# Kernel optimization log

Hardware: AMD Instinct MI355X
Metric: run time of the kernel (lower is better)

## Reference

```python
import jax, jax.numpy as jnp
import numpy as np

DIMS = (50000, 50000)
ORDER = len(DIMS)
NUM_FEATS = 64
QLEVEL = 4
Q = 1 << QLEVEL
V = 1 << ORDER                      # number of corners (2^order)
N_QUERIES = 1_000_000
WHICH_AXIS = np.repeat(np.arange(ORDER), DIMS)          # [sum(dims)]
OFFSETS = np.concatenate([[0], np.cumsum(DIMS)[:-1]])   # row offset of each axis in feats
# corner bit table: flattening of a [2]*order grid is row-major, so axis i's bit is (v >> (ORDER-1-i)) & 1
VBITS = (np.arange(V)[:, None] >> (ORDER - 1 - np.arange(ORDER))[None, :]) & 1  # [V, ORDER]


def setup_inputs() -> dict:
    key = jax.random.key(0)
    k = jax.random.split(key, 8)
    S = sum(DIMS)
    init_scale = 0.01 / NUM_FEATS ** 0.5
    values = jax.random.truncated_normal(k[0], -2.0, 2.0, (1, V, NUM_FEATS), dtype=jnp.float32) * init_scale
    feats = jax.random.uniform(k[1], (S, NUM_FEATS), dtype=jnp.float32)
    lo = 1.0 / (1 << (QLEVEL + 1))
    cand_row = jnp.linspace(lo, 1.0 - lo, Q, dtype=jnp.float32).reshape(1, 1, Q)
    candidates = jnp.tile(cand_row, (ORDER, NUM_FEATS, 1))
    scale = jnp.zeros((1,), jnp.float32)
    bias = jnp.zeros((1,), jnp.float32)
    idx0 = jax.random.randint(k[2], (N_QUERIES,), 0, DIMS[0])
    idx1 = jax.random.randint(k[3], (N_QUERIES,), 0, DIMS[1])
    return {"values": values, "feats": feats, "candidates": candidates,
            "scale": scale, "bias": bias, "idx0": idx0, "idx1": idx1}


def reference(values, feats, candidates, scale, bias, idx0, idx1):
    # --- prepare_inputs: straight-through quantization of feats ---
    target_keys = candidates[WHICH_AXIS]                                  # [S, F, Q]
    assigned = jnp.argmin(jnp.abs(feats[:, :, None] - target_keys), -1)   # [S, F]
    qkeys = jnp.take_along_axis(target_keys, assigned[:, :, None], -1)[..., 0]  # [S, F]
    probs = qkeys + feats - jax.lax.stop_gradient(feats)                  # STE
    p = jnp.stack([probs, 1.0 - probs], 0)                                # [2, S, F]

    # --- per-axis gathers ---
    idxs = [idx0, idx1]
    gathers = [p[:, OFFSETS[i] + idxs[i]] for i in range(ORDER)]          # each [2, N, F]

    # --- corner-wise outer product across axes ---
    corner = gathers[0][VBITS[:, 0]]                                      # [V, N, F]
    for i in range(1, ORDER):
        corner = corner * gathers[i][VBITS[:, i]]

    # --- contraction with corner values, halve features, tanh gate ---
    t = jnp.einsum('vf,vnf->nf', values[0], corner)                       # [N, F]
    half = NUM_FEATS // 2
    a = t[:, :half].sum(-1)                                               # [N]
    b = t[:, half:].sum(-1)                                               # [N]
    return a * jnp.tanh(b) * jnp.exp(scale[0]) + bias[0]
```

## Files before the change

### kernel.cpp

```cpp
#include <hip/hip_runtime.h>
#include <stdint.h>

#define NF    64
#define DIM0  50000
#define SROWS 100000
#define TPB   256
#define QPT   2
#define COEF_OFF_BYTES (SROWS * 32)

typedef float    f32x4 __attribute__((ext_vector_type(4)));
typedef uint32_t u32x4 __attribute__((ext_vector_type(4)));

__global__ void quantize_kernel(const float* __restrict__ feats,
                                const float* __restrict__ values,
                                uint32_t* __restrict__ qcodes,
                                float* __restrict__ coef) {
    int t = threadIdx.x;
    if (blockIdx.x == 0 && t < NF) {
        float v0 = values[t], v1 = values[NF + t];
        float v2 = values[2 * NF + t], v3 = values[3 * NF + t];
        float W = v0 - v1 - v2 + v3;
        float X = v1 - v3, Y = v2 - v3;
        float Wp = W * (1.0f / 256.0f);
        float Xp = W * (1.0f / 512.0f) + X * (1.0f / 16.0f);
        float Yp = W * (1.0f / 512.0f) + Y * (1.0f / 16.0f);
        float C  = W * (1.0f / 1024.0f) + (X + Y) * (1.0f / 32.0f) + v3;
        ((f32x4*)coef)[t] = (f32x4){Wp, Xp, Yp, C};
        float Cs = C;
        Cs += __shfl_xor(Cs, 1);  Cs += __shfl_xor(Cs, 2);
        Cs += __shfl_xor(Cs, 4);  Cs += __shfl_xor(Cs, 8);
        Cs += __shfl_xor(Cs, 16);
        if (t == 0)  coef[NF * 4 + 0] = Cs;
        if (t == 32) coef[NF * 4 + 1] = Cs;
    }

    int gid = blockIdx.x * blockDim.x + t;
    const f32x4* fr = (const f32x4*)(feats + (size_t)gid * 8);
    f32x4 fA = __builtin_nontemporal_load(fr);
    f32x4 fB = __builtin_nontemporal_load(fr + 1);
    float fv[8] = {fA.x, fA.y, fA.z, fA.w, fB.x, fB.y, fB.z, fB.w};

    uint32_t word = 0u;
#pragma unroll
    for (int j = 0; j < 8; ++j) {
        float x = fmaf(fv[j], 16.0f, -1.0f);
        int q = (int)ceilf(x);
        q = q < 0 ? 0 : (q > 15 ? 15 : q);
        word |= (uint32_t)q << (4 * j);
    }
    __builtin_nontemporal_store(word, qcodes + gid);
}

__global__ __launch_bounds__(TPB) void query_kernel(
        const uint32_t* __restrict__ qcodes,
        const f32x4* __restrict__ coef,
        const float* __restrict__ scale,
        const float* __restrict__ bias,
        const int* __restrict__ idx0,
        const int* __restrict__ idx1,
        float* __restrict__ out, int N) {
    int t = threadIdx.x;
    int base = blockIdx.x * (TPB * QPT) + t;

    uint32_t aw[QPT][8], bw[QPT][8];
#pragma unroll
    for (int k = 0; k < QPT; ++k) {
        int n = base + k * TPB;
        int m = n < N ? n : N - 1;
        int r0 = __builtin_nontemporal_load(idx0 + m);
        int r1 = DIM0 + __builtin_nontemporal_load(idx1 + m);
        const u32x4* pa = (const u32x4*)(qcodes + (size_t)r0 * 8);
        const u32x4* pb = (const u32x4*)(qcodes + (size_t)r1 * 8);
        u32x4 x0 = pa[0], x1 = pa[1];
        u32x4 y0 = pb[0], y1 = pb[1];
        aw[k][0] = x0.x; aw[k][1] = x0.y; aw[k][2] = x0.z; aw[k][3] = x0.w;
        aw[k][4] = x1.x; aw[k][5] = x1.y; aw[k][6] = x1.z; aw[k][7] = x1.w;
        bw[k][0] = y0.x; bw[k][1] = y0.y; bw[k][2] = y0.z; bw[k][3] = y0.w;
        bw[k][4] = y1.x; bw[k][5] = y1.y; bw[k][6] = y1.z; bw[k][7] = y1.w;
    }

    float a1[QPT] = {0.f, 0.f};
    float b1[QPT] = {0.f, 0.f};
#pragma unroll
    for (int wd = 0; wd < 8; ++wd) {
#pragma unroll
        for (int j = 0; j < 8; ++j) {
            int f = wd * 8 + j;
            f32x4 c = coef[f];
#pragma unroll
            for (int k = 0; k < QPT; ++k) {
                float A = (float)((aw[k][wd] >> (4 * j)) & 15u);
                float B = (float)((bw[k][wd] >> (4 * j)) & 15u);
                float h = fmaf(c.x, B, c.y);
                float g = fmaf(c.z, B, (wd < 4 ? a1[k] : b1[k]));
                if (wd < 4) a1[k] = fmaf(A, h, g);
                else        b1[k] = fmaf(A, h, g);
            }
        }
    }

    const float* cs = (const float*)coef;
    float Ca = cs[NF * 4 + 0];
    float Cb = cs[NF * 4 + 1];
    float es = expf(scale[0]);
    float bi = bias[0];
#pragma unroll
    for (int k = 0; k < QPT; ++k) {
        int n = base + k * TPB;
        if (n < N) {
            float asum = a1[k] + Ca;
            float bsum = b1[k] + Cb;
            __builtin_nontemporal_store(asum * tanhf(bsum) * es + bi, out + n);
        }
    }
}

extern "C" void kernel_launch(void* const* d_in, const int* in_sizes, int n_in,
                              void* d_out, int out_size, void* d_ws, size_t ws_size,
                              hipStream_t stream) {
    const float* values = (const float*)d_in[0];
    const float* feats  = (const float*)d_in[1];
    const float* scale  = (const float*)d_in[3];
    const float* bias   = (const float*)d_in[4];
    const int*   idx0   = (const int*)d_in[5];
    const int*   idx1   = (const int*)d_in[6];
    float*       out    = (float*)d_out;

    uint32_t* qcodes = (uint32_t*)d_ws;
    float*    coef   = (float*)((char*)d_ws + COEF_OFF_BYTES);

    int nwords = SROWS * 8;
    quantize_kernel<<<nwords / TPB, TPB, 0, stream>>>(feats, values, qcodes, coef);

    int N = out_size;
    int qblocks = (N + TPB * QPT - 1) / (TPB * QPT);
    query_kernel<<<qblocks, TPB, 0, stream>>>(
        qcodes, (const f32x4*)coef, scale, bias, idx0, idx1, out, N);
}
```

Measured before the change: 44.79 us.

## Bucket queries by idx0 block and stage axis-0 codes in LDS

Adds a counting sort of queries by idx0>>8: a histogram fused into the quantize kernel, a serial prefix kernel and a scatter kernel that writes packed (n, low row bits, idx1) records. The query kernel then loads 256 axis-0 code rows per bucket into LDS and serves axis-0 gathers from there, leaving only the axis-1 gather in global memory. The goal is to remove random global gathers for one axis. In exchange it adds three more launches, a memset, atomics and a record array written and read back, and the output writes become scattered.

```diff
diff --git a/kernel.cpp b/kernel.cpp
--- a/kernel.cpp
+++ b/kernel.cpp
@@ -1,117 +1,198 @@
 #include <hip/hip_runtime.h>
 #include <stdint.h>
 
-#define NF    64
-#define DIM0  50000
-#define SROWS 100000
-#define TPB   256
-#define QPT   2
-#define COEF_OFF_BYTES (SROWS * 32)
+#define NF     64
+#define DIM0   50000
+#define SROWS  100000
+#define TPB    256
+#define NB     196
+#define KSPLIT 8
+#define QBLKS  3125
+
+#define OFF_CODES 0u
+#define OFF_COEF  3200000u
+#define OFF_CNT   3201536u
+#define OFF_BASE  3202560u
+#define OFF_CUR   3203584u
+#define OFF_REC   3204608u
 
 typedef float    f32x4 __attribute__((ext_vector_type(4)));
 typedef uint32_t u32x4 __attribute__((ext_vector_type(4)));
-
-__global__ void quantize_kernel(const float* __restrict__ feats,
-                                const float* __restrict__ values,
-                                uint32_t* __restrict__ qcodes,
-                                float* __restrict__ coef) {
+typedef uint32_t u32x2 __attribute__((ext_vector_type(2)));
+
+__global__ __launch_bounds__(TPB) void quanthist_kernel(
+        const float* __restrict__ feats, const float* __restrict__ values,
+        const int* __restrict__ idx0,
+        uint32_t* __restrict__ qcodes, float* __restrict__ coef,
+        uint32_t* __restrict__ gcnt, int N) {
+    int bid = blockIdx.x;
+    int t   = threadIdx.x;
+
+    if (bid < QBLKS) {
+        if (bid == 0 && t < NF) {
+            float v0 = values[t], v1 = values[NF + t];
+            float v2 = values[2 * NF + t], v3 = values[3 * NF + t];
+            float W = v0 - v1 - v2 + v3;
+            float X = v1 - v3, Y = v2 - v3;
+            float Wp = W * (1.0f / 256.0f);
+            float Xp = W * (1.0f / 512.0f) + X * (1.0f / 16.0f);
+            float Yp = W * (1.0f / 512.0f) + Y * (1.0f / 16.0f);
+            float C  = W * (1.0f / 1024.0f) + (X + Y) * (1.0f / 32.0f) + v3;
+            ((f32x4*)coef)[t] = (f32x4){Wp, Xp, Yp, C};
+            float Cs = C;
+            Cs += __shfl_xor(Cs, 1);  Cs += __shfl_xor(Cs, 2);
+            Cs += __shfl_xor(Cs, 4);  Cs += __shfl_xor(Cs, 8);
+            Cs += __shfl_xor(Cs, 16);
+            if (t == 0)  coef[NF * 4 + 0] = Cs;
+            if (t == 32) coef[NF * 4 + 1] = Cs;
+        }
+        int gid = bid * TPB + t;
+        const f32x4* fr = (const f32x4*)(feats + (size_t)gid * 8);
+        f32x4 fA = __builtin_nontemporal_load(fr);
+        f32x4 fB = __builtin_nontemporal_load(fr + 1);
+        float fv[8] = {fA.x, fA.y, fA.z, fA.w, fB.x, fB.y, fB.z, fB.w};
+        uint32_t word = 0u;
+#pragma unroll
+        for (int j = 0; j < 8; ++j) {
+            float x = fmaf(fv[j], 16.0f, -1.0f);
+            int q = (int)ceilf(x);
+            q = q < 0 ? 0 : (q > 15 ? 15 : q);
+            word |= (uint32_t)q << (4 * j);
+        }
+        qcodes[gid] = word;
+    } else {
+        __shared__ uint32_t scnt[NB];
+        for (int i = t; i < NB; i += TPB) scnt[i] = 0;
+        __syncthreads();
+        int q0 = (bid - QBLKS) * 1024;
+#pragma unroll
+        for (int k = 0; k < 4; ++k) {
+            int n = q0 + k * TPB + t;
+            if (n < N) atomicAdd(&scnt[(uint32_t)idx0[n] >> 8], 1u);
+        }
+        __syncthreads();
+        for (int i = t; i < NB; i += TPB)
+            if (scnt[i]) atomicAdd(&gcnt[i], scnt[i]);
+    }
+}
+
+__global__ void prefix_kernel(const uint32_t* __restrict__ cnt,
+                              uint32_t* __restrict__ base,
+                              uint32_t* __restrict__ cursor) {
+    if (threadIdx.x == 0 && blockIdx.x == 0) {
+        uint32_t acc = 0;
+        for (int i = 0; i < NB; ++i) {
+            base[i] = acc; cursor[i] = acc; acc += cnt[i];
+        }
+        base[NB] = acc;
+    }
+}
+
+__global__ __launch_bounds__(TPB) void scatter_kernel(
+        const int* __restrict__ idx0, const int* __restrict__ idx1,
+        uint32_t* __restrict__ cursor, uint2* __restrict__ rec, int N) {
+    __shared__ uint32_t scnt[NB];
+    __shared__ uint32_t sstart[NB];
     int t = threadIdx.x;
-    if (blockIdx.x == 0 && t < NF) {
-        float v0 = values[t], v1 = values[NF + t];
-        float v2 = values[2 * NF + t], v3 = values[3 * NF + t];
-        float W = v0 - v1 - v2 + v3;
-        float X = v1 - v3, Y = v2 - v3;
-        float Wp = W * (1.0f / 256.0f);
-        float Xp = W * (1.0f / 512.0f) + X * (1.0f / 16.0f);
-        float Yp = W * (1.0f / 512.0f) + Y * (1.0f / 16.0f);
-        float C  = W * (1.0f / 1024.0f) + (X + Y) * (1.0f / 32.0f) + v3;
-        ((f32x4*)coef)[t] = (f32x4){Wp, Xp, Yp, C};
-        float Cs = C;
-        Cs += __shfl_xor(Cs, 1);  Cs += __shfl_xor(Cs, 2);
-        Cs += __shfl_xor(Cs, 4);  Cs += __shfl_xor(Cs, 8);
-        Cs += __shfl_xor(Cs, 16);
-        if (t == 0)  coef[NF * 4 + 0] = Cs;
-        if (t == 32) coef[NF * 4 + 1] = Cs;
-    }
-
-    int gid = blockIdx.x * blockDim.x + t;
-    const f32x4* fr = (const f32x4*)(feats + (size_t)gid * 8);
-    f32x4 fA = __builtin_nontemporal_load(fr);
-    f32x4 fB = __builtin_nontemporal_load(fr + 1);
-    float fv[8] = {fA.x, fA.y, fA.z, fA.w, fB.x, fB.y, fB.z, fB.w};
-
-    uint32_t word = 0u;
-#pragma unroll
-    for (int j = 0; j < 8; ++j) {
-        float x = fmaf(fv[j], 16.0f, -1.0f);
-        int q = (int)ceilf(x);
-        q = q < 0 ? 0 : (q > 15 ? 15 : q);
-        word |= (uint32_t)q << (4 * j);
-    }
-    __builtin_nontemporal_store(word, qcodes + gid);
-}
-
-__global__ __launch_bounds__(TPB) void query_kernel(
+    for (int i = t; i < NB; i += TPB) scnt[i] = 0;
+    __syncthreads();
+
+    int q0 = blockIdx.x * 1024;
+    int r0v[4], r1v[4], bk[4];
+#pragma unroll
+    for (int k = 0; k < 4; ++k) {
+        int n = q0 + k * TPB + t;
+        if (n < N) {
+            r0v[k] = __builtin_nontemporal_load(idx0 + n);
+            r1v[k] = __builtin_nontemporal_load(idx1 + n);
+            bk[k] = (uint32_t)r0v[k] >> 8;
+            atomicAdd(&scnt[bk[k]], 1u);
+        } else bk[k] = -1;
+    }
+    __syncthreads();
+    for (int i = t; i < NB; i += TPB) {
+        uint32_t c = scnt[i];
+        sstart[i] = c ? atomicAdd(&cursor[i], c) : 0u;
+    }
+    __syncthreads();
+    for (int i = t; i < NB; i += TPB) scnt[i] = 0;
+    __syncthreads();
+#pragma unroll
+    for (int k = 0; k < 4; ++k) {
+        if (bk[k] >= 0) {
+            int n = q0 + k * TPB + t;
+            uint32_t r = atomicAdd(&scnt[bk[k]], 1u);
+            uint32_t pos = sstart[bk[k]] + r;
+            rec[pos] = make_uint2((uint32_t)n | ((uint32_t)(r0v[k] & 255) << 20),
+                                  (uint32_t)r1v[k]);
+        }
+    }
+}
+
+__global__ __launch_bounds__(TPB) void bquery_kernel(
         const uint32_t* __restrict__ qcodes,
+        const uint2* __restrict__ rec,
+        const uint32_t* __restrict__ base,
         const f32x4* __restrict__ coef,
         const float* __restrict__ scale,
         const float* __restrict__ bias,
-        const int* __restrict__ idx0,
-        const int* __restrict__ idx1,
-        float* __restrict__ out, int N) {
+        float* __restrict__ out) {
+    __shared__ uint32_t lds[256 * 8];
+    int b = blockIdx.x / KSPLIT;
+    int k = blockIdx.x % KSPLIT;
     int t = threadIdx.x;
-    int base = blockIdx.x * (TPB * QPT) + t;
-
-    uint32_t aw[QPT][8], bw[QPT][8];
-#pragma unroll
-    for (int k = 0; k < QPT; ++k) {
-        int n = base + k * TPB;
-        int m = n < N ? n : N - 1;
-        int r0 = __builtin_nontemporal_load(idx0 + m);
-        int r1 = DIM0 + __builtin_nontemporal_load(idx1 + m);
-        const u32x4* pa = (const u32x4*)(qcodes + (size_t)r0 * 8);
-        const u32x4* pb = (const u32x4*)(qcodes + (size_t)r1 * 8);
-        u32x4 x0 = pa[0], x1 = pa[1];
-        u32x4 y0 = pb[0], y1 = pb[1];
-        aw[k][0] = x0.x; aw[k][1] = x0.y; aw[k][2] = x0.z; aw[k][3] = x0.w;
-        aw[k][4] = x1.x; aw[k][5] = x1.y; aw[k][6] = x1.z; aw[k][7] = x1.w;
-        bw[k][0] = y0.x; bw[k][1] = y0.y; bw[k][2] = y0.z; bw[k][3] = y0.w;
-        bw[k][4] = y1.x; bw[k][5] = y1.y; bw[k][6] = y1.z; bw[k][7] = y1.w;
-    }
-
-    float a1[QPT] = {0.f, 0.f};
-    float b1[QPT] = {0.f, 0.f};
-#pragma unroll
-    for (int wd = 0; wd < 8; ++wd) {
-#pragma unroll
-        for (int j = 0; j < 8; ++j) {
-            int f = wd * 8 + j;
-            f32x4 c = coef[f];
-#pragma unroll
-            for (int k = 0; k < QPT; ++k) {
-                float A = (float)((aw[k][wd] >> (4 * j)) & 15u);
-                float B = (float)((bw[k][wd] >> (4 * j)) & 15u);
-                float h = fmaf(c.x, B, c.y);
-                float g = fmaf(c.z, B, (wd < 4 ? a1[k] : b1[k]));
-                if (wd < 4) a1[k] = fmaf(A, h, g);
-                else        b1[k] = fmaf(A, h, g);
-            }
-        }
-    }
-
+
+    int row0  = b * 256;
+    int nrows = min(256, DIM0 - row0);
+    int words = nrows * 8;
+    for (int i = t; i < words; i += TPB)
+        lds[i] = qcodes[(size_t)row0 * 8 + i];
+
+    uint32_t s = base[b], e = base[b + 1];
+    __syncthreads();
+
+    uint32_t len   = e - s;
+    uint32_t chunk = (len + KSPLIT - 1) / KSPLIT;
+    uint32_t start = s + (uint32_t)k * chunk;
+    uint32_t end   = min(start + chunk, e);
+
+    float es = expf(scale[0]);
+    float bi = bias[0];
     const float* cs = (const float*)coef;
     float Ca = cs[NF * 4 + 0];
     float Cb = cs[NF * 4 + 1];
-    float es = expf(scale[0]);
-    float bi = bias[0];
-#pragma unroll
-    for (int k = 0; k < QPT; ++k) {
-        int n = base + k * TPB;
-        if (n < N) {
-            float asum = a1[k] + Ca;
-            float bsum = b1[k] + Cb;
-            __builtin_nontemporal_store(asum * tanhf(bsum) * es + bi, out + n);
-        }
+
+    for (uint32_t i = start + t; i < end; i += TPB) {
+        u32x2 rc = __builtin_nontemporal_load((const u32x2*)(rec + i));
+        uint32_t n    = rc.x & 0xFFFFFu;
+        uint32_t r0lo = (rc.x >> 20) & 0xFFu;
+        uint32_t r1   = rc.y;
+
+        const uint32_t* ar = &lds[r0lo * 8];
+        uint32_t aw[8];
+#pragma unroll
+        for (int w = 0; w < 8; ++w) aw[w] = ar[w];
+        const u32x4* pb = (const u32x4*)(qcodes + ((size_t)DIM0 + r1) * 8);
+        u32x4 y0 = pb[0], y1 = pb[1];
+        uint32_t bw[8] = {y0.x, y0.y, y0.z, y0.w, y1.x, y1.y, y1.z, y1.w};
+
+        float a1 = 0.f, b1 = 0.f;
+#pragma unroll
+        for (int wd = 0; wd < 8; ++wd) {
+#pragma unroll
+            for (int j = 0; j < 8; ++j) {
+                int f = wd * 8 + j;
+                f32x4 c = coef[f];
+                float A = (float)((aw[wd] >> (4 * j)) & 15u);
+                float B = (float)((bw[wd] >> (4 * j)) & 15u);
+                float h = fmaf(c.x, B, c.y);
+                float g = fmaf(c.z, B, (wd < 4 ? a1 : b1));
+                if (wd < 4) a1 = fmaf(A, h, g);
+                else        b1 = fmaf(A, h, g);
+            }
+        }
+        float res = (a1 + Ca) * tanhf(b1 + Cb) * es + bi;
+        __builtin_nontemporal_store(res, out + n);
     }
 }
 
@@ -126,14 +207,22 @@
     const int*   idx1   = (const int*)d_in[6];
     float*       out    = (float*)d_out;
 
-    uint32_t* qcodes = (uint32_t*)d_ws;
-    float*    coef   = (float*)((char*)d_ws + COEF_OFF_BYTES);
-
-    int nwords = SROWS * 8;
-    quantize_kernel<<<nwords / TPB, TPB, 0, stream>>>(feats, values, qcodes, coef);
+    char* ws = (char*)d_ws;
+    uint32_t* qcodes = (uint32_t*)(ws + OFF_CODES);
+    float*    coef   = (float*)   (ws + OFF_COEF);
+    uint32_t* gcnt   = (uint32_t*)(ws + OFF_CNT);
+    uint32_t* gbase  = (uint32_t*)(ws + OFF_BASE);
+    uint32_t* gcur   = (uint32_t*)(ws + OFF_CUR);
+    uint2*    rec    = (uint2*)   (ws + OFF_REC);
 
     int N = out_size;
-    int qblocks = (N + TPB * QPT - 1) / (TPB * QPT);
-    query_kernel<<<qblocks, TPB, 0, stream>>>(
-        qcodes, (const f32x4*)coef, scale, bias, idx0, idx1, out, N);
-}
+    int hblks = (N + 1023) / 1024;
+
+    hipMemsetAsync(gcnt, 0, NB * sizeof(uint32_t), stream);
+    quanthist_kernel<<<QBLKS + hblks, TPB, 0, stream>>>(
+        feats, values, idx0, qcodes, coef, gcnt, N);
+    prefix_kernel<<<1, 64, 0, stream>>>(gcnt, gbase, gcur);
+    scatter_kernel<<<hblks, TPB, 0, stream>>>(idx0, idx1, gcur, rec, N);
+    bquery_kernel<<<NB * KSPLIT, TPB, 0, stream>>>(
+        qcodes, rec, gbase, (const f32x4*)coef, scale, bias, out);
+}
```

Measured after the change: 112.1 us. 2.5x slower.

## Bucket queries by idx0 range before gathering to improve cache locality

Applied to the files above, without the earlier changes.

Adds a scatter pass that sorts queries into 8 buckets by idx0 row range, writing packed (query id, r0, r1) records. The query kernel then processes each bucket in chunks so the idx0-side code rows in flight stay within a small slice, aiming for better L2/MALL reuse. In exchange it adds a memset, an extra kernel launch, a global atomic and a write plus read of 8 MB of records, and the output writes become scattered. The qcodes table is only about 3.2 MB, so it may already fit in cache.

```diff
diff --git a/kernel.cpp b/kernel.cpp
--- a/kernel.cpp
+++ b/kernel.cpp
@@ -1,20 +1,27 @@
 #include <hip/hip_runtime.h>
 #include <stdint.h>
 
-#define NF    64
-#define DIM0  50000
-#define SROWS 100000
-#define TPB   256
-#define QPT   2
-#define COEF_OFF_BYTES (SROWS * 32)
+#define NF     64
+#define DIM0   50000
+#define SROWS  100000
+#define TPB    256
+#define NBKT   8
+#define BROWS  6250
+#define CAP    160000u
+#define NCH    512
+#define QBLKS  3125
+
+#define OFF_CODES 0u
+#define OFF_COEF  3200000u
+#define OFF_CUR   3202048u
+#define OFF_REC   3203072u
 
 typedef float    f32x4 __attribute__((ext_vector_type(4)));
 typedef uint32_t u32x4 __attribute__((ext_vector_type(4)));
 
-__global__ void quantize_kernel(const float* __restrict__ feats,
-                                const float* __restrict__ values,
-                                uint32_t* __restrict__ qcodes,
-                                float* __restrict__ coef) {
+__global__ __launch_bounds__(TPB) void quantize_kernel(
+        const float* __restrict__ feats, const float* __restrict__ values,
+        uint32_t* __restrict__ qcodes, float* __restrict__ coef) {
     int t = threadIdx.x;
     if (blockIdx.x == 0 && t < NF) {
         float v0 = values[t], v1 = values[NF + t];
@@ -34,7 +41,7 @@
         if (t == 32) coef[NF * 4 + 1] = Cs;
     }
 
-    int gid = blockIdx.x * blockDim.x + t;
+    int gid = blockIdx.x * TPB + t;
     const f32x4* fr = (const f32x4*)(feats + (size_t)gid * 8);
     f32x4 fA = __builtin_nontemporal_load(fr);
     f32x4 fB = __builtin_nontemporal_load(fr + 1);
@@ -48,70 +55,96 @@
         q = q < 0 ? 0 : (q > 15 ? 15 : q);
         word |= (uint32_t)q << (4 * j);
     }
-    __builtin_nontemporal_store(word, qcodes + gid);
+    qcodes[gid] = word;
 }
 
-__global__ __launch_bounds__(TPB) void query_kernel(
+__global__ __launch_bounds__(TPB) void scatter_kernel(
+        const int* __restrict__ idx0, const int* __restrict__ idx1,
+        uint32_t* __restrict__ cursor, uint2* __restrict__ rec, int N) {
+    __shared__ uint32_t scnt[NBKT], sstart[NBKT];
+    int t = threadIdx.x;
+    if (t < NBKT) scnt[t] = 0;
+    __syncthreads();
+
+    int q0 = blockIdx.x * 1024;
+    int r0v[4], r1v[4], bk[4];
+    uint32_t rk[4];
+#pragma unroll
+    for (int k = 0; k < 4; ++k) {
+        int n = q0 + k * TPB + t;
+        if (n < N) {
+            r0v[k] = __builtin_nontemporal_load(idx0 + n);
+            r1v[k] = __builtin_nontemporal_load(idx1 + n);
+            bk[k]  = (uint32_t)r0v[k] / BROWS;
+            rk[k]  = atomicAdd(&scnt[bk[k]], 1u);
+        } else bk[k] = -1;
+    }
+    __syncthreads();
+    if (t < NBKT) sstart[t] = scnt[t] ? atomicAdd(&cursor[t], scnt[t]) : 0u;
+    __syncthreads();
+#pragma unroll
+    for (int k = 0; k < 4; ++k) {
+        if (bk[k] >= 0) {
+            int n = q0 + k * TPB + t;
+            uint32_t pos = (uint32_t)bk[k] * CAP + sstart[bk[k]] + rk[k];
+            rec[pos] = make_uint2((uint32_t)n,
+                                  ((uint32_t)r0v[k] << 16) | (uint32_t)r1v[k]);
+        }
+    }
+}
+
+__global__ __launch_bounds__(TPB) void bquery_kernel(
         const uint32_t* __restrict__ qcodes,
+        const uint2* __restrict__ rec,
+        const uint32_t* __restrict__ cursor,
         const f32x4* __restrict__ coef,
         const float* __restrict__ scale,
         const float* __restrict__ bias,
-        const int* __restrict__ idx0,
-        const int* __restrict__ idx1,
-        float* __restrict__ out, int N) {
-    int t = threadIdx.x;
-    int base = blockIdx.x * (TPB * QPT) + t;
+        float* __restrict__ out) {
+    int b  = blockIdx.x & (NBKT - 1);
+    int ch = blockIdx.x >> 3;
 
-    uint32_t aw[QPT][8], bw[QPT][8];
-#pragma unroll
-    for (int k = 0; k < QPT; ++k) {
-        int n = base + k * TPB;
-        int m = n < N ? n : N - 1;
-        int r0 = __builtin_nontemporal_load(idx0 + m);
-        int r1 = DIM0 + __builtin_nontemporal_load(idx1 + m);
-        const u32x4* pa = (const u32x4*)(qcodes + (size_t)r0 * 8);
-        const u32x4* pb = (const u32x4*)(qcodes + (size_t)r1 * 8);
-        u32x4 x0 = pa[0], x1 = pa[1];
-        u32x4 y0 = pb[0], y1 = pb[1];
-        aw[k][0] = x0.x; aw[k][1] = x0.y; aw[k][2] = x0.z; aw[k][3] = x0.w;
-        aw[k][4] = x1.x; aw[k][5] = x1.y; aw[k][6] = x1.z; aw[k][7] = x1.w;
-        bw[k][0] = y0.x; bw[k][1] = y0.y; bw[k][2] = y0.z; bw[k][3] = y0.w;
-        bw[k][4] = y1.x; bw[k][5] = y1.y; bw[k][6] = y1.z; bw[k][7] = y1.w;
-    }
-
-    float a1[QPT] = {0.f, 0.f};
-    float b1[QPT] = {0.f, 0.f};
-#pragma unroll
-    for (int wd = 0; wd < 8; ++wd) {
-#pragma unroll
-        for (int j = 0; j < 8; ++j) {
-            int f = wd * 8 + j;
-            f32x4 c = coef[f];
-#pragma unroll
-            for (int k = 0; k < QPT; ++k) {
-                float A = (float)((aw[k][wd] >> (4 * j)) & 15u);
-                float B = (float)((bw[k][wd] >> (4 * j)) & 15u);
-                float h = fmaf(c.x, B, c.y);
-                float g = fmaf(c.z, B, (wd < 4 ? a1[k] : b1[k]));
-                if (wd < 4) a1[k] = fmaf(A, h, g);
-                else        b1[k] = fmaf(A, h, g);
-            }
-        }
-    }
+    uint32_t cnt = min(cursor[b], CAP);
+    uint32_t per = (cnt + NCH - 1) / NCH;
+    uint32_t s   = min(per * (uint32_t)ch, cnt);
+    uint32_t e   = min(s + per, cnt);
+    uint32_t rbase = (uint32_t)b * CAP;
 
     const float* cs = (const float*)coef;
     float Ca = cs[NF * 4 + 0];
     float Cb = cs[NF * 4 + 1];
     float es = expf(scale[0]);
     float bi = bias[0];
+
+    for (uint32_t i = s + threadIdx.x; i < e; i += TPB) {
+        uint2 rc = rec[rbase + i];
+        uint32_t n  = rc.x;
+        uint32_t r0 = rc.y >> 16;
+        uint32_t r1 = rc.y & 0xFFFFu;
+
+        const u32x4* pa = (const u32x4*)(qcodes + (size_t)r0 * 8);
+        const u32x4* pb = (const u32x4*)(qcodes + ((size_t)DIM0 + r1) * 8);
+        u32x4 x0 = pa[0], x1 = pa[1];
+        u32x4 y0 = pb[0], y1 = pb[1];
+        uint32_t aw[8] = {x0.x, x0.y, x0.z, x0.w, x1.x, x1.y, x1.z, x1.w};
+        uint32_t bw[8] = {y0.x, y0.y, y0.z, y0.w, y1.x, y1.y, y1.z, y1.w};
+
+        float a1 = 0.f, b1 = 0.f;
 #pragma unroll
-    for (int k = 0; k < QPT; ++k) {
-        int n = base + k * TPB;
-        if (n < N) {
-            float asum = a1[k] + Ca;
-            float bsum = b1[k] + Cb;
-            __builtin_nontemporal_store(asum * tanhf(bsum) * es + bi, out + n);
+        for (int wd = 0; wd < 8; ++wd) {
+#pragma unroll
+            for (int j = 0; j < 8; ++j) {
+                int f = wd * 8 + j;
+                f32x4 c = coef[f];
+                float A = (float)((aw[wd] >> (4 * j)) & 15u);
+                float B = (float)((bw[wd] >> (4 * j)) & 15u);
+                float h = fmaf(c.x, B, c.y);
+                float g = fmaf(c.z, B, (wd < 4 ? a1 : b1));
+                if (wd < 4) a1 = fmaf(A, h, g);
+                else        b1 = fmaf(A, h, g);
+            }
         }
+        out[n] = (a1 + Ca) * tanhf(b1 + Cb) * es + bi;
     }
 }
 
@@ -126,14 +159,18 @@
     const int*   idx1   = (const int*)d_in[6];
     float*       out    = (float*)d_out;
 
-    uint32_t* qcodes = (uint32_t*)d_ws;
-    float*    coef   = (float*)((char*)d_ws + COEF_OFF_BYTES);
-
-    int nwords = SROWS * 8;
-    quantize_kernel<<<nwords / TPB, TPB, 0, stream>>>(feats, values, qcodes, coef);
+    char* ws = (char*)d_ws;
+    uint32_t* qcodes = (uint32_t*)(ws + OFF_CODES);
+    float*    coef   = (float*)   (ws + OFF_COEF);
+    uint32_t* gcur   = (uint32_t*)(ws + OFF_CUR);
+    uint2*    rec    = (uint2*)   (ws + OFF_REC);
 
     int N = out_size;
-    int qblocks = (N + TPB * QPT - 1) / (TPB * QPT);
-    query_kernel<<<qblocks, TPB, 0, stream>>>(
-        qcodes, (const f32x4*)coef, scale, bias, idx0, idx1, out, N);
+    int sblks = (N + 1023) / 1024;
+
+    hipMemsetAsync(gcur, 0, NBKT * sizeof(uint32_t), stream);
+    quantize_kernel<<<QBLKS, TPB, 0, stream>>>(feats, values, qcodes, coef);
+    scatter_kernel<<<sblks, TPB, 0, stream>>>(idx0, idx1, gcur, rec, N);
+    bquery_kernel<<<NBKT * NCH, TPB, 0, stream>>>(
+        qcodes, rec, gcur, (const f32x4*)coef, scale, bias, out);
 }
```

Measured after the change: 65.57 us. 1.46x slower.
